# Kernel tuning notes

Hardware: AMD Instinct MI355X
Metric: run time of the kernel (lower is better)

Reference implementation:

```python
import jax, jax.numpy as jnp
import numpy as np

DOF = 7
DT = 0.1
MAX_VEL = 20.0
ACTION_RANGE = 50.0
BATCH = 16384


def skew(w):
    x, y, z = w[..., 0], w[..., 1], w[..., 2]
    o = jnp.zeros_like(x)
    return jnp.stack([jnp.stack([o, -z, y], -1),
                      jnp.stack([z, o, -x], -1),
                      jnp.stack([-y, x, o], -1)], -2)


def exp6(xi):
    # xi: (..., 6) twist [omega, v] (angular first). General se(3) exponential.
    w, v = xi[..., :3], xi[..., 3:]
    th = jnp.linalg.norm(w, axis=-1)                     # (...)
    small = th < 1e-10
    th_s = jnp.where(small, 1.0, th)
    W = skew(w / th_s[..., None])
    W2 = W @ W
    s, c = jnp.sin(th), jnp.cos(th)
    I3 = jnp.eye(3, dtype=xi.dtype)
    R = I3 + s[..., None, None] * W + (1.0 - c)[..., None, None] * W2
    Gm = th[..., None, None] * I3 + (1.0 - c)[..., None, None] * W + (th - s)[..., None, None] * W2
    p = jnp.einsum('...ij,...j->...i', Gm, v / th_s[..., None])
    R = jnp.where(small[..., None, None], I3, R)
    p = jnp.where(small[..., None], v, p)
    top = jnp.concatenate([R, p[..., None]], -1)
    bot = jnp.broadcast_to(jnp.array([0., 0., 0., 1.], xi.dtype), top.shape[:-2] + (1, 4))
    return jnp.concatenate([top, bot], -2)


def trans_inv(T):
    R = T[..., :3, :3]
    p = T[..., :3, 3]
    Rt = jnp.swapaxes(R, -1, -2)
    pi = -jnp.einsum('...ij,...j->...i', Rt, p)
    top = jnp.concatenate([Rt, pi[..., None]], -1)
    bot = jnp.broadcast_to(jnp.array([0., 0., 0., 1.], T.dtype), top.shape[:-2] + (1, 4))
    return jnp.concatenate([top, bot], -2)


def adjoint(T):
    R = T[..., :3, :3]
    p = T[..., :3, 3]
    pR = skew(p) @ R
    z = jnp.zeros_like(R)
    return jnp.concatenate([jnp.concatenate([R, z], -1),
                            jnp.concatenate([pR, R], -1)], -2)


def ad(V):
    w, v = V[..., :3], V[..., 3:]
    W, Vm = skew(w), skew(v)
    z = jnp.zeros_like(W)
    return jnp.concatenate([jnp.concatenate([W, z], -1),
                            jnp.concatenate([Vm, W], -1)], -2)


def inverse_dynamics(q, dq, ddq, gravity, ftip, Mlist, Glist, A):
    # Newton-Euler inverse dynamics (Modern Robotics), batched over B.
    B, n = q.shape
    dt = q.dtype
    V = jnp.zeros((B, 6), dt)
    Vd = jnp.concatenate([jnp.zeros((B, 3), dt), -jnp.broadcast_to(gravity, (B, 3))], -1)
    AdTs, Vs, Vds = [], [], []
    for i in range(n):  # forward recursion over joints (small fixed dof)
        Ti = exp6(-A[i] * q[:, i, None]) @ trans_inv(Mlist[i])   # (B,4,4)
        AdTi = adjoint(Ti)                                       # (B,6,6)
        V = jnp.einsum('bij,bj->bi', AdTi, V) + A[i] * dq[:, i, None]
        Vd = (jnp.einsum('bij,bj->bi', AdTi, Vd) + A[i] * ddq[:, i, None]
              + jnp.einsum('bij,j->bi', ad(V), A[i]) * dq[:, i, None])
        AdTs.append(AdTi)
        Vs.append(V)
        Vds.append(Vd)
    AdTs.append(jnp.broadcast_to(adjoint(trans_inv(Mlist[n])), (B, 6, 6)))
    F = jnp.broadcast_to(ftip, (B, 6))
    taus = [None] * n
    for i in range(n - 1, -1, -1):  # backward recursion
        GV = jnp.einsum('ij,bj->bi', Glist[i], Vs[i])
        F = (jnp.einsum('bji,bj->bi', AdTs[i + 1], F)
             + jnp.einsum('ij,bj->bi', Glist[i], Vds[i])
             - jnp.einsum('bji,bj->bi', ad(Vs[i]), GV))
        taus[i] = jnp.sum(F * A[i], -1)
    return jnp.stack(taus, -1)  # (B, n)


def forward_dynamics(q, dq, tau, gravity, ftip, Mlist, Glist, A):
    n = q.shape[1]
    z = jnp.zeros_like(q)
    g0 = jnp.zeros(3, q.dtype)
    f0 = jnp.zeros(6, q.dtype)
    # mass matrix columns via unit-ddq inverse dynamics
    cols = jax.vmap(lambda e: inverse_dynamics(q, z, jnp.broadcast_to(e, q.shape),
                                               g0, f0, Mlist, Glist, A))(jnp.eye(n, dtype=q.dtype))
    Mmat = jnp.transpose(cols, (1, 2, 0))                        # (B,n,n)
    # coriolis + gravity + end-effector bias in one pass (ddq=0)
    h = inverse_dynamics(q, dq, z, gravity, ftip, Mlist, Glist, A)
    return jnp.linalg.solve(Mmat, (tau - h)[..., None])[..., 0]


def _forward(state, torque, M_param, A, G_param, gravity, ftip):
    n = DOF
    # M property: keep top 3 rows, force bottom row to [0,0,0,1]
    bot = jnp.broadcast_to(jnp.array([0., 0., 0., 1.], M_param.dtype), (n + 1, 1, 4))
    Mlist = jnp.concatenate([M_param[:, :3], bot], axis=1)       # (n+1,4,4)
    # G property: diag(Ixx,Iyy,Izz,m,m,m)
    dvec = jnp.concatenate([G_param[:, :3], jnp.repeat(G_param[:, 3:4], 3, axis=1)], -1)
    Glist = dvec[:, :, None] * jnp.eye(6, dtype=G_param.dtype)   # (n,6,6)
    tau = torque * ACTION_RANGE

    def derivs(s, t):
        qpos, qvel, qf = s[..., :n], s[..., n:2 * n], s[..., 2 * n:3 * n]
        qacc = forward_dynamics(qpos, qvel, qf, gravity, ftip, Mlist, Glist, A)
        return jnp.concatenate([qvel, qacc, jnp.zeros_like(qf)], -1)

    s0 = jnp.concatenate([state, tau], -1)
    dt = DT
    k1 = derivs(s0, 0.0)
    k2 = derivs(s0 + 0.5 * dt * k1, 0.5 * dt)
    k3 = derivs(s0 + 0.5 * dt * k2, 0.5 * dt)
    k4 = derivs(s0 + dt * k3, dt)
    s1 = s0 + (dt / 6.0) * (k1 + 2.0 * k2 + 2.0 * k3 + k4)
    ns = s1[..., :2 * n]
    q = (ns[..., :n] + jnp.pi) % (2.0 * jnp.pi) - jnp.pi
    dq = jnp.clip(ns[..., n:], -MAX_VEL, MAX_VEL)
    # fk_in_space: chain link transforms, last frame is end-effector
    B = q.shape[0]
    T = jnp.broadcast_to(jnp.eye(4, dtype=q.dtype), (B, 4, 4))
    for i in range(n):
        T = T @ Mlist[i] @ exp6(A[i] * q[:, i, None])
    T = T @ Mlist[n]
    ee = T[:, :3, 3]
    return jnp.concatenate([q, dq], -1), ee


def setup_inputs() -> dict:
    key = jax.random.key(0)
    ks = jax.random.split(key, 6)
    state = jax.random.normal(ks[0], (BATCH, 2 * DOF), jnp.float32)
    torque = jax.random.normal(ks[1], (BATCH, DOF), jnp.float32)
    M_param = jnp.eye(4, dtype=jnp.float32)[None] + 0.05 * jax.random.normal(ks[2], (DOF + 1, 4, 4), jnp.float32)
    A = jax.random.uniform(ks[3], (DOF, 6), jnp.float32)
    G_param = jax.random.uniform(ks[4], (DOF, 4), jnp.float32, minval=0.1, maxval=1.0)
    gravity = jnp.array([0.0, -9.8, 0.0], jnp.float32)
    ftip = jnp.zeros(6, jnp.float32)
    return {"state": state, "torque": torque, "M_param": M_param, "A": A,
            "G_param": G_param, "gravity": gravity, "ftip": ftip}


def reference(state, torque, M_param, A, G_param, gravity, ftip):
    return _forward(state, torque, M_param, A, G_param, gravity, ftip)
```

## Files before the change

kernel.cpp:

```cpp
#include <hip/hip_runtime.h>
#include <math.h>

#define NB 16384

struct SConsts {
  float MrT[8][9];
  float mp[8][3];
  float A[7][6];
  float Gd[7][6];
  float X7p[3];
  float g[3];
  float ftip[6];
};

__device__ __forceinline__ void syncw() {
  __builtin_amdgcn_sched_barrier(0);
  __builtin_amdgcn_wave_barrier();
  __builtin_amdgcn_sched_barrier(0);
}

__device__ __forceinline__ float dot6(const float* a, const float* b) {
  return a[0]*b[0]+a[1]*b[1]+a[2]*b[2]+a[3]*b[3]+a[4]*b[4]+a[5]*b[5];
}

__device__ __forceinline__ void exp6_dev(float wx, float wy, float wz,
                                         float vx, float vy, float vz,
                                         float R[9], float p[3]) {
  float th2 = wx*wx + wy*wy + wz*wz;
  float th  = __builtin_amdgcn_sqrtf(th2);
  bool sm = th < 1e-10f;
  float ths = sm ? 1.0f : th;
  float inv = __builtin_amdgcn_rcpf(ths);
  float ux = wx*inv, uy = wy*inv, uz = wz*inv;
  float s = __sinf(th);
  float c = __cosf(th);
  float omc = 1.0f - c;
  float r00 = c + omc*ux*ux;
  float r01 = omc*ux*uy - s*uz;
  float r02 = omc*ux*uz + s*uy;
  float r10 = omc*uy*ux + s*uz;
  float r11 = c + omc*uy*uy;
  float r12 = omc*uy*uz - s*ux;
  float r20 = omc*uz*ux - s*uy;
  float r21 = omc*uz*uy + s*ux;
  float r22 = c + omc*uz*uz;
  float k1 = omc*inv, k2 = (th - s)*inv;
  float cx = uy*vz - uz*vy, cy = uz*vx - ux*vz, cz = ux*vy - uy*vx;
  float udv = ux*vx + uy*vy + uz*vz;
  float px = vx + k1*cx + k2*(ux*udv - vx);
  float py = vy + k1*cy + k2*(uy*udv - vy);
  float pz = vz + k1*cz + k2*(uz*udv - vz);
  R[0]=sm?1.f:r00; R[1]=sm?0.f:r01; R[2]=sm?0.f:r02;
  R[3]=sm?0.f:r10; R[4]=sm?1.f:r11; R[5]=sm?0.f:r12;
  R[6]=sm?0.f:r20; R[7]=sm?0.f:r21; R[8]=sm?1.f:r22;
  p[0]=sm?vx:px; p[1]=sm?vy:py; p[2]=sm?vz:pz;
}

__device__ __forceinline__ void Xapply(const float* R, const float* p,
                                       const float in[6], float out[6]) {
  float a = R[0]*in[0]+R[1]*in[1]+R[2]*in[2];
  float b = R[3]*in[0]+R[4]*in[1]+R[5]*in[2];
  float c = R[6]*in[0]+R[7]*in[1]+R[8]*in[2];
  float d = R[0]*in[3]+R[1]*in[4]+R[2]*in[5];
  float e = R[3]*in[3]+R[4]*in[4]+R[5]*in[5];
  float f = R[6]*in[3]+R[7]*in[4]+R[8]*in[5];
  out[0]=a; out[1]=b; out[2]=c;
  out[3] = p[1]*c - p[2]*b + d;
  out[4] = p[2]*a - p[0]*c + e;
  out[5] = p[0]*b - p[1]*a + f;
}

__device__ __forceinline__ void XTapply(const float* R, const float* p,
                                        const float in[6], float out[6]) {
  float fx=in[3], fy=in[4], fz=in[5];
  float tx = in[0] - (p[1]*fz - p[2]*fy);
  float ty = in[1] - (p[2]*fx - p[0]*fz);
  float tz = in[2] - (p[0]*fy - p[1]*fx);
  out[0] = R[0]*tx + R[3]*ty + R[6]*tz;
  out[1] = R[1]*tx + R[4]*ty + R[7]*tz;
  out[2] = R[2]*tx + R[5]*ty + R[8]*tz;
  out[3] = R[0]*fx + R[3]*fy + R[6]*fz;
  out[4] = R[1]*fx + R[4]*fy + R[7]*fz;
  out[5] = R[2]*fx + R[5]*fy + R[8]*fz;
}

extern "C" __global__ void __launch_bounds__(64, 2)
arm_kernel(const float* __restrict__ state, const float* __restrict__ torque,
           const float* __restrict__ Mp, const float* __restrict__ Ain,
           const float* __restrict__ Gp, const float* __restrict__ grav,
           const float* __restrict__ ftip_in, float* __restrict__ out)
{
  __shared__ SConsts C;
  __shared__ float XL[8][100];
  __shared__ float CL[8][68];
  const int t = threadIdx.x;

  {
    int i = t >> 3;
    #pragma unroll
    for (int kk = (t & 7); kk < 12; kk += 8) {
      if (kk < 9) {
        int r = kk / 3, c = kk - 3*(kk/3);
        C.MrT[i][c*3 + r] = Mp[i*16 + r*4 + c];
      } else {
        int r = kk - 9;
        C.mp[i][r] = Mp[i*16 + r*4 + 3];
      }
    }
    if (t < 42) {
      int i2 = t / 6, k = t - 6*(t/6);
      C.A[i2][k] = Ain[t];
      C.Gd[i2][k] = (k < 3) ? Gp[i2*4 + k] : Gp[i2*4 + 3];
    }
    if (t < 3) C.g[t] = grav[t];
    if (t < 6) C.ftip[t] = ftip_in[t];
  }
  syncw();
  if (t < 3)
    C.X7p[t] = -(C.MrT[7][t*3+0]*C.mp[7][0] + C.MrT[7][t*3+1]*C.mp[7][1] + C.MrT[7][t*3+2]*C.mp[7][2]);
  syncw();

  const int sub = t & 7;
  const int e   = t >> 3;
  const int b   = blockIdx.x * 8 + e;
  const int subc = (sub < 7) ? sub : 6;

  float dq0[7], tau[7], dqs[7];
  #pragma unroll
  for (int k = 0; k < 7; ++k) {
    dq0[k] = state[b*14 + 7 + k];
    tau[k] = torque[b*7 + k] * 50.0f;
    dqs[k] = dq0[k];
  }
  float q0s  = state[b*14 + subc];
  float dq0s = dq0[0];
  #pragma unroll
  for (int k = 1; k < 7; ++k) dq0s = (subc == k) ? dq0[k] : dq0s;

  float qss = q0s, dqss = dq0s;
  float accqs = 0.0f, accdqs = 0.0f;
  float a[7];
  const float gm = (sub == 7) ? 1.0f : 0.0f;

  #pragma unroll 1
  for (int stage = 0; stage < 4; ++stage) {
    syncw();
    if (sub < 7) {
      float Re[9], pe[3];
      exp6_dev(-C.A[sub][0]*qss, -C.A[sub][1]*qss, -C.A[sub][2]*qss,
               -C.A[sub][3]*qss, -C.A[sub][4]*qss, -C.A[sub][5]*qss, Re, pe);
      float Xr[12];
      #pragma unroll
      for (int r = 0; r < 3; ++r) {
        #pragma unroll
        for (int c = 0; c < 3; ++c)
          Xr[r*3+c] = Re[r*3+0]*C.MrT[sub][0+c] + Re[r*3+1]*C.MrT[sub][3+c] + Re[r*3+2]*C.MrT[sub][6+c];
      }
      #pragma unroll
      for (int r = 0; r < 3; ++r)
        Xr[9+r] = pe[r] - (Xr[r*3+0]*C.mp[sub][0] + Xr[r*3+1]*C.mp[sub][1] + Xr[r*3+2]*C.mp[sub][2]);
      float4* dst = (float4*)&XL[e][sub*12];
      dst[0] = make_float4(Xr[0],Xr[1],Xr[2],Xr[3]);
      dst[1] = make_float4(Xr[4],Xr[5],Xr[6],Xr[7]);
      dst[2] = make_float4(Xr[8],Xr[9],Xr[10],Xr[11]);
    }
    syncw();

    float X[7][12];
    #pragma unroll
    for (int i = 0; i < 7; ++i) {
      const float4* sx = (const float4*)&XL[e][i*12];
      float4 x0 = sx[0], x1 = sx[1], x2 = sx[2];
      X[i][0]=x0.x; X[i][1]=x0.y; X[i][2]=x0.z; X[i][3]=x0.w;
      X[i][4]=x1.x; X[i][5]=x1.y; X[i][6]=x1.z; X[i][7]=x1.w;
      X[i][8]=x2.x; X[i][9]=x2.y; X[i][10]=x2.z; X[i][11]=x2.w;
    }

    float V[6] = {0,0,0,0,0,0};
    float Vd[6];
    Vd[0]=0.0f; Vd[1]=0.0f; Vd[2]=0.0f;
    Vd[3] = -gm*C.g[0]; Vd[4] = -gm*C.g[1]; Vd[5] = -gm*C.g[2];
    float Fb[7][6];
    #pragma unroll
    for (int i = 0; i < 7; ++i) {
      float dqi  = (sub == 7) ? dqs[i] : 0.0f;
      float ddqi = (sub == i) ? 1.0f : 0.0f;
      float tv[6];
      Xapply(X[i], X[i]+9, V, tv);
      #pragma unroll
      for (int k = 0; k < 6; ++k) V[k] = tv[k] + C.A[i][k]*dqi;
      Xapply(X[i], X[i]+9, Vd, tv);
      float wx=V[0],wy=V[1],wz=V[2],vx=V[3],vy=V[4],vz=V[5];
      float ax=C.A[i][0],ay=C.A[i][1],az=C.A[i][2];
      float bx=C.A[i][3],by=C.A[i][4],bz=C.A[i][5];
      Vd[0] = tv[0] + ax*ddqi + (wy*az - wz*ay)*dqi;
      Vd[1] = tv[1] + ay*ddqi + (wz*ax - wx*az)*dqi;
      Vd[2] = tv[2] + az*ddqi + (wx*ay - wy*ax)*dqi;
      Vd[3] = tv[3] + bx*ddqi + (vy*az - vz*ay + wy*bz - wz*by)*dqi;
      Vd[4] = tv[4] + by*ddqi + (vz*ax - vx*az + wz*bx - wx*bz)*dqi;
      Vd[5] = tv[5] + bz*ddqi + (vx*ay - vy*ax + wx*by - wy*bx)*dqi;
      float g0=C.Gd[i][0], g1=C.Gd[i][1], g2=C.Gd[i][2], m=C.Gd[i][3];
      float Gt0=g0*wx, Gt1=g1*wy, Gt2=g2*wz;
      float Gb0=m*vx,  Gb1=m*vy,  Gb2=m*vz;
      Fb[i][0] = g0*Vd[0] + (wy*Gt2 - wz*Gt1) + (vy*Gb2 - vz*Gb1);
      Fb[i][1] = g1*Vd[1] + (wz*Gt0 - wx*Gt2) + (vz*Gb0 - vx*Gb2);
      Fb[i][2] = g2*Vd[2] + (wx*Gt1 - wy*Gt0) + (vx*Gb1 - vy*Gb0);
      Fb[i][3] = m*Vd[3] + (wy*Gb2 - wz*Gb1);
      Fb[i][4] = m*Vd[4] + (wz*Gb0 - wx*Gb2);
      Fb[i][5] = m*Vd[5] + (wx*Gb1 - wy*Gb0);
    }
    float col[7];
    float F[6];
    #pragma unroll
    for (int k = 0; k < 6; ++k) F[k] = gm*C.ftip[k];
    #pragma unroll
    for (int i = 6; i >= 0; --i) {
      float tv[6];
      if (i == 6) XTapply(C.MrT[7], C.X7p, F, tv);
      else        XTapply(X[i+1], X[i+1]+9, F, tv);
      #pragma unroll
      for (int k = 0; k < 6; ++k) F[k] = tv[k] + Fb[i][k];
      col[i] = dot6(F, C.A[i]);
    }

    syncw();
    #pragma unroll
    for (int k = 0; k < 7; ++k) CL[e][k*8 + sub] = col[k];
    syncw();
    float Mm[7][7], rhs[7];
    #pragma unroll
    for (int i = 0; i < 7; ++i) {
      const float4* rp = (const float4*)&CL[e][i*8];
      float4 r0 = rp[0], r1 = rp[1];
      Mm[i][0]=r0.x; Mm[i][1]=r0.y; Mm[i][2]=r0.z; Mm[i][3]=r0.w;
      Mm[i][4]=r1.x; Mm[i][5]=r1.y; Mm[i][6]=r1.z;
      rhs[i] = tau[i] - r1.w;
    }

    float invd[7];
    #pragma unroll
    for (int k = 0; k < 7; ++k) {
      invd[k] = __builtin_amdgcn_rcpf(Mm[k][k]);
      #pragma unroll
      for (int i2 = k+1; i2 < 7; ++i2) {
        float f = Mm[i2][k] * invd[k];
        #pragma unroll
        for (int c2 = k+1; c2 < 7; ++c2) Mm[i2][c2] -= f * Mm[k][c2];
        rhs[i2] -= f * rhs[k];
      }
    }
    #pragma unroll
    for (int i2 = 6; i2 >= 0; --i2) {
      float s = rhs[i2];
      #pragma unroll
      for (int c2 = i2+1; c2 < 7; ++c2) s -= Mm[i2][c2] * a[c2];
      a[i2] = s * invd[i2];
    }

    float a_own = a[0];
    #pragma unroll
    for (int k = 1; k < 7; ++k) a_own = (subc == k) ? a[k] : a_own;
    float w = (stage == 1 || stage == 2) ? 2.0f : 1.0f;
    accqs  += w*dqss;
    accdqs += w*a_own;
    if (stage < 3) {
      float cc = (stage == 2) ? 0.1f : 0.05f;
      qss  = q0s + cc*dqss;
      dqss = dq0s + cc*a_own;
      #pragma unroll
      for (int k = 0; k < 7; ++k) dqs[k] = dq0[k] + cc*a[k];
    }
  }

  const float c6 = (float)(0.1/6.0);
  const float PI_F = 3.14159265358979323846f;
  const float TWO_PI_F = 6.28318530717958647692f;
  const float INV_TWO_PI_F = 0.15915494309189535f;
  float q1 = q0s  + c6*accqs;
  float d1 = dq0s + c6*accdqs;
  float x = q1 + PI_F;
  float n = floorf(x * INV_TWO_PI_F);
  float y = fmaf(n, -TWO_PI_F, x);
  y = (y < 0.0f) ? y + TWO_PI_F : y;
  y = (y >= TWO_PI_F) ? y - TWO_PI_F : y;
  float qw_own  = y - PI_F;
  float dqw_own = fminf(fmaxf(d1, -20.0f), 20.0f);
  if (sub < 7) {
    out[b*14 + sub]     = qw_own;
    out[b*14 + 7 + sub] = dqw_own;
  }

  syncw();
  if (sub < 7) {
    float Re[9], pe[3];
    exp6_dev(C.A[sub][0]*qw_own, C.A[sub][1]*qw_own, C.A[sub][2]*qw_own,
             C.A[sub][3]*qw_own, C.A[sub][4]*qw_own, C.A[sub][5]*qw_own, Re, pe);
    float L[12];
    #pragma unroll
    for (int r = 0; r < 3; ++r) {
      #pragma unroll
      for (int c = 0; c < 3; ++c)
        L[r*3+c] = C.MrT[sub][0*3+r]*Re[0*3+c] + C.MrT[sub][1*3+r]*Re[1*3+c] + C.MrT[sub][2*3+r]*Re[2*3+c];
      L[9+r] = C.MrT[sub][0*3+r]*pe[0] + C.MrT[sub][1*3+r]*pe[1] + C.MrT[sub][2*3+r]*pe[2] + C.mp[sub][r];
    }
    float4* dst = (float4*)&XL[e][sub*12];
    dst[0] = make_float4(L[0],L[1],L[2],L[3]);
    dst[1] = make_float4(L[4],L[5],L[6],L[7]);
    dst[2] = make_float4(L[8],L[9],L[10],L[11]);
  }
  syncw();
  float X2[7][12];
  #pragma unroll
  for (int i = 0; i < 7; ++i) {
    const float4* sx = (const float4*)&XL[e][i*12];
    float4 x0 = sx[0], x1 = sx[1], x2 = sx[2];
    X2[i][0]=x0.x; X2[i][1]=x0.y; X2[i][2]=x0.z; X2[i][3]=x0.w;
    X2[i][4]=x1.x; X2[i][5]=x1.y; X2[i][6]=x1.z; X2[i][7]=x1.w;
    X2[i][8]=x2.x; X2[i][9]=x2.y; X2[i][10]=x2.z; X2[i][11]=x2.w;
  }
  float v0 = C.mp[7][0], v1 = C.mp[7][1], v2 = C.mp[7][2];
  #pragma unroll
  for (int i = 6; i >= 0; --i) {
    float n0 = X2[i][0]*v0 + X2[i][1]*v1 + X2[i][2]*v2 + X2[i][9];
    float n1 = X2[i][3]*v0 + X2[i][4]*v1 + X2[i][5]*v2 + X2[i][10];
    float n2 = X2[i][6]*v0 + X2[i][7]*v1 + X2[i][8]*v2 + X2[i][11];
    v0 = n0; v1 = n1; v2 = n2;
  }
  {
    float ev = v0;
    ev = (sub == 1) ? v1 : ev;
    ev = (sub == 2) ? v2 : ev;
    if (sub < 3) out[NB*14 + b*3 + sub] = ev;
  }
}

extern "C" void kernel_launch(void* const* d_in, const int* in_sizes, int n_in,
                              void* d_out, int out_size, void* d_ws, size_t ws_size,
                              hipStream_t stream) {
  const float* state  = (const float*)d_in[0];
  const float* torque = (const float*)d_in[1];
  const float* Mp     = (const float*)d_in[2];
  const float* Ain    = (const float*)d_in[3];
  const float* Gp     = (const float*)d_in[4];
  const float* grav   = (const float*)d_in[5];
  const float* ftip   = (const float*)d_in[6];
  float* out = (float*)d_out;
  hipLaunchKernelGGL(arm_kernel, dim3(NB/8), dim3(64), 0, stream,
                     state, torque, Mp, Ain, Gp, grav, ftip, out);
}
```

Measured before the change: 26.53 us.

## Map each arm column to its own wavefront with 64 batch elements per block

Restructures the thread mapping so that each of 8 wavefronts handles one mass-matrix column (or the bias term) for 64 batch elements. Before, 8 lanes of one wave cooperated on a single element. Because every lane in a wave now takes the same path, the column waves can run a specialised cheaper recursion that drops the velocity terms, and only wave 7 runs the full Newton-Euler with gravity and velocities. Divergent per-lane masking goes away, but the change brings block-wide __syncthreads, larger LDS use (about 47KB), and more per-wave register pressure. The end-effector FK now runs on one wave only.

After: 30.60 us. 15.3% more time.

```diff
diff --git a/kernel.cpp b/kernel.cpp
--- a/kernel.cpp
+++ b/kernel.cpp
@@ -2,6 +2,7 @@
 #include <math.h>
 
 #define NB 16384
+#define ESTR 92
 
 struct SConsts {
   float MrT[8][9];
@@ -12,12 +13,6 @@
   float g[3];
   float ftip[6];
 };
-
-__device__ __forceinline__ void syncw() {
-  __builtin_amdgcn_sched_barrier(0);
-  __builtin_amdgcn_wave_barrier();
-  __builtin_amdgcn_sched_barrier(0);
-}
 
 __device__ __forceinline__ float dot6(const float* a, const float* b) {
   return a[0]*b[0]+a[1]*b[1]+a[2]*b[2]+a[3]*b[3]+a[4]*b[4]+a[5]*b[5];
@@ -84,18 +79,65 @@
   out[5] = R[2]*fx + R[5]*fy + R[8]*fz;
 }
 
-extern "C" __global__ void __launch_bounds__(64, 2)
+__device__ __forceinline__ void build_X(const SConsts& C, int j, float q,
+                                        float* dstp) {
+  float Re[9], pe[3];
+  exp6_dev(-C.A[j][0]*q, -C.A[j][1]*q, -C.A[j][2]*q,
+           -C.A[j][3]*q, -C.A[j][4]*q, -C.A[j][5]*q, Re, pe);
+  float Xr[12];
+  #pragma unroll
+  for (int r = 0; r < 3; ++r) {
+    #pragma unroll
+    for (int c = 0; c < 3; ++c)
+      Xr[r*3+c] = Re[r*3+0]*C.MrT[j][0+c] + Re[r*3+1]*C.MrT[j][3+c] + Re[r*3+2]*C.MrT[j][6+c];
+  }
+  #pragma unroll
+  for (int r = 0; r < 3; ++r)
+    Xr[9+r] = pe[r] - (Xr[r*3+0]*C.mp[j][0] + Xr[r*3+1]*C.mp[j][1] + Xr[r*3+2]*C.mp[j][2]);
+  float4* dst = (float4*)dstp;
+  dst[0] = make_float4(Xr[0],Xr[1],Xr[2],Xr[3]);
+  dst[1] = make_float4(Xr[4],Xr[5],Xr[6],Xr[7]);
+  dst[2] = make_float4(Xr[8],Xr[9],Xr[10],Xr[11]);
+}
+
+__device__ __forceinline__ void solve7(float Mm[7][7], float rhs[7], float a[7]) {
+  float invd[7];
+  #pragma unroll
+  for (int k = 0; k < 7; ++k) {
+    invd[k] = __builtin_amdgcn_rcpf(Mm[k][k]);
+    #pragma unroll
+    for (int i2 = k+1; i2 < 7; ++i2) {
+      float f = Mm[i2][k] * invd[k];
+      #pragma unroll
+      for (int c2 = k+1; c2 < 7; ++c2) Mm[i2][c2] -= f * Mm[k][c2];
+      rhs[i2] -= f * rhs[k];
+    }
+  }
+  #pragma unroll
+  for (int i2 = 6; i2 >= 0; --i2) {
+    float s = rhs[i2];
+    #pragma unroll
+    for (int c2 = i2+1; c2 < 7; ++c2) s -= Mm[i2][c2] * a[c2];
+    a[i2] = s * invd[i2];
+  }
+}
+
+extern "C" __global__ void __launch_bounds__(512, 2)
 arm_kernel(const float* __restrict__ state, const float* __restrict__ torque,
            const float* __restrict__ Mp, const float* __restrict__ Ain,
            const float* __restrict__ Gp, const float* __restrict__ grav,
            const float* __restrict__ ftip_in, float* __restrict__ out)
 {
   __shared__ SConsts C;
-  __shared__ float XL[8][100];
-  __shared__ float CL[8][68];
+  __shared__ float XL[64*ESTR];
+  __shared__ float CL[64*ESTR];
   const int t = threadIdx.x;
-
-  {
+  const int w = t >> 6;
+  const int l = t & 63;
+  const int b = blockIdx.x * 64 + l;
+  const int wc = (w < 7) ? w : 6;
+
+  if (t < 64) {
     int i = t >> 3;
     #pragma unroll
     for (int kk = (t & 7); kk < 12; kk += 8) {
@@ -115,100 +157,89 @@
     if (t < 3) C.g[t] = grav[t];
     if (t < 6) C.ftip[t] = ftip_in[t];
   }
-  syncw();
+  __syncthreads();
   if (t < 3)
     C.X7p[t] = -(C.MrT[7][t*3+0]*C.mp[7][0] + C.MrT[7][t*3+1]*C.mp[7][1] + C.MrT[7][t*3+2]*C.mp[7][2]);
-  syncw();
-
-  const int sub = t & 7;
-  const int e   = t >> 3;
-  const int b   = blockIdx.x * 8 + e;
-  const int subc = (sub < 7) ? sub : 6;
-
-  float dq0[7], tau[7], dqs[7];
-  #pragma unroll
-  for (int k = 0; k < 7; ++k) {
-    dq0[k] = state[b*14 + 7 + k];
-    tau[k] = torque[b*7 + k] * 50.0f;
-    dqs[k] = dq0[k];
-  }
-  float q0s  = state[b*14 + subc];
-  float dq0s = dq0[0];
-  #pragma unroll
-  for (int k = 1; k < 7; ++k) dq0s = (subc == k) ? dq0[k] : dq0s;
+
+  float tau[7];
+  #pragma unroll
+  for (int k = 0; k < 7; ++k) tau[k] = torque[b*7 + k] * 50.0f;
+  float q0s  = state[b*14 + wc];
+  float dq0s = state[b*14 + 7 + wc];
+  float dq0[7], dqs[7];
+  if (w == 7) {
+    #pragma unroll
+    for (int k = 0; k < 7; ++k) { dq0[k] = state[b*14 + 7 + k]; dqs[k] = dq0[k]; }
+  }
 
   float qss = q0s, dqss = dq0s;
-  float accqs = 0.0f, accdqs = 0.0f;
+  float accq = 0.0f, accdq = 0.0f;
   float a[7];
-  const float gm = (sub == 7) ? 1.0f : 0.0f;
+  const float gm = (w == 7) ? 1.0f : 0.0f;
 
   #pragma unroll 1
   for (int stage = 0; stage < 4; ++stage) {
-    syncw();
-    if (sub < 7) {
-      float Re[9], pe[3];
-      exp6_dev(-C.A[sub][0]*qss, -C.A[sub][1]*qss, -C.A[sub][2]*qss,
-               -C.A[sub][3]*qss, -C.A[sub][4]*qss, -C.A[sub][5]*qss, Re, pe);
-      float Xr[12];
-      #pragma unroll
-      for (int r = 0; r < 3; ++r) {
-        #pragma unroll
-        for (int c = 0; c < 3; ++c)
-          Xr[r*3+c] = Re[r*3+0]*C.MrT[sub][0+c] + Re[r*3+1]*C.MrT[sub][3+c] + Re[r*3+2]*C.MrT[sub][6+c];
-      }
-      #pragma unroll
-      for (int r = 0; r < 3; ++r)
-        Xr[9+r] = pe[r] - (Xr[r*3+0]*C.mp[sub][0] + Xr[r*3+1]*C.mp[sub][1] + Xr[r*3+2]*C.mp[sub][2]);
-      float4* dst = (float4*)&XL[e][sub*12];
-      dst[0] = make_float4(Xr[0],Xr[1],Xr[2],Xr[3]);
-      dst[1] = make_float4(Xr[4],Xr[5],Xr[6],Xr[7]);
-      dst[2] = make_float4(Xr[8],Xr[9],Xr[10],Xr[11]);
-    }
-    syncw();
+    if (w < 7) build_X(C, w, qss, &XL[l*ESTR + w*12]);
+    __syncthreads();
 
     float X[7][12];
     #pragma unroll
     for (int i = 0; i < 7; ++i) {
-      const float4* sx = (const float4*)&XL[e][i*12];
+      const float4* sx = (const float4*)&XL[l*ESTR + i*12];
       float4 x0 = sx[0], x1 = sx[1], x2 = sx[2];
       X[i][0]=x0.x; X[i][1]=x0.y; X[i][2]=x0.z; X[i][3]=x0.w;
       X[i][4]=x1.x; X[i][5]=x1.y; X[i][6]=x1.z; X[i][7]=x1.w;
       X[i][8]=x2.x; X[i][9]=x2.y; X[i][10]=x2.z; X[i][11]=x2.w;
     }
 
-    float V[6] = {0,0,0,0,0,0};
-    float Vd[6];
-    Vd[0]=0.0f; Vd[1]=0.0f; Vd[2]=0.0f;
-    Vd[3] = -gm*C.g[0]; Vd[4] = -gm*C.g[1]; Vd[5] = -gm*C.g[2];
     float Fb[7][6];
-    #pragma unroll
-    for (int i = 0; i < 7; ++i) {
-      float dqi  = (sub == 7) ? dqs[i] : 0.0f;
-      float ddqi = (sub == i) ? 1.0f : 0.0f;
-      float tv[6];
-      Xapply(X[i], X[i]+9, V, tv);
-      #pragma unroll
-      for (int k = 0; k < 6; ++k) V[k] = tv[k] + C.A[i][k]*dqi;
-      Xapply(X[i], X[i]+9, Vd, tv);
-      float wx=V[0],wy=V[1],wz=V[2],vx=V[3],vy=V[4],vz=V[5];
-      float ax=C.A[i][0],ay=C.A[i][1],az=C.A[i][2];
-      float bx=C.A[i][3],by=C.A[i][4],bz=C.A[i][5];
-      Vd[0] = tv[0] + ax*ddqi + (wy*az - wz*ay)*dqi;
-      Vd[1] = tv[1] + ay*ddqi + (wz*ax - wx*az)*dqi;
-      Vd[2] = tv[2] + az*ddqi + (wx*ay - wy*ax)*dqi;
-      Vd[3] = tv[3] + bx*ddqi + (vy*az - vz*ay + wy*bz - wz*by)*dqi;
-      Vd[4] = tv[4] + by*ddqi + (vz*ax - vx*az + wz*bx - wx*bz)*dqi;
-      Vd[5] = tv[5] + bz*ddqi + (vx*ay - vy*ax + wx*by - wy*bx)*dqi;
-      float g0=C.Gd[i][0], g1=C.Gd[i][1], g2=C.Gd[i][2], m=C.Gd[i][3];
-      float Gt0=g0*wx, Gt1=g1*wy, Gt2=g2*wz;
-      float Gb0=m*vx,  Gb1=m*vy,  Gb2=m*vz;
-      Fb[i][0] = g0*Vd[0] + (wy*Gt2 - wz*Gt1) + (vy*Gb2 - vz*Gb1);
-      Fb[i][1] = g1*Vd[1] + (wz*Gt0 - wx*Gt2) + (vz*Gb0 - vx*Gb2);
-      Fb[i][2] = g2*Vd[2] + (wx*Gt1 - wy*Gt0) + (vx*Gb1 - vy*Gb0);
-      Fb[i][3] = m*Vd[3] + (wy*Gb2 - wz*Gb1);
-      Fb[i][4] = m*Vd[4] + (wz*Gb0 - wx*Gb2);
-      Fb[i][5] = m*Vd[5] + (wx*Gb1 - wy*Gb0);
-    }
+    if (w == 7) {
+      float V[6] = {0,0,0,0,0,0};
+      float Vd[6];
+      Vd[0]=0.0f; Vd[1]=0.0f; Vd[2]=0.0f;
+      Vd[3] = -C.g[0]; Vd[4] = -C.g[1]; Vd[5] = -C.g[2];
+      #pragma unroll
+      for (int i = 0; i < 7; ++i) {
+        float dqi = dqs[i];
+        float tv[6];
+        Xapply(X[i], X[i]+9, V, tv);
+        #pragma unroll
+        for (int k = 0; k < 6; ++k) V[k] = tv[k] + C.A[i][k]*dqi;
+        Xapply(X[i], X[i]+9, Vd, tv);
+        float wx=V[0],wy=V[1],wz=V[2],vx=V[3],vy=V[4],vz=V[5];
+        float ax=C.A[i][0],ay=C.A[i][1],az=C.A[i][2];
+        float bx=C.A[i][3],by=C.A[i][4],bz=C.A[i][5];
+        Vd[0] = tv[0] + (wy*az - wz*ay)*dqi;
+        Vd[1] = tv[1] + (wz*ax - wx*az)*dqi;
+        Vd[2] = tv[2] + (wx*ay - wy*ax)*dqi;
+        Vd[3] = tv[3] + (vy*az - vz*ay + wy*bz - wz*by)*dqi;
+        Vd[4] = tv[4] + (vz*ax - vx*az + wz*bx - wx*bz)*dqi;
+        Vd[5] = tv[5] + (vx*ay - vy*ax + wx*by - wy*bx)*dqi;
+        float g0=C.Gd[i][0], g1=C.Gd[i][1], g2=C.Gd[i][2], m=C.Gd[i][3];
+        float Gt0=g0*wx, Gt1=g1*wy, Gt2=g2*wz;
+        float Gb0=m*vx,  Gb1=m*vy,  Gb2=m*vz;
+        Fb[i][0] = g0*Vd[0] + (wy*Gt2 - wz*Gt1) + (vy*Gb2 - vz*Gb1);
+        Fb[i][1] = g1*Vd[1] + (wz*Gt0 - wx*Gt2) + (vz*Gb0 - vx*Gb2);
+        Fb[i][2] = g2*Vd[2] + (wx*Gt1 - wy*Gt0) + (vx*Gb1 - vy*Gb0);
+        Fb[i][3] = m*Vd[3] + (wy*Gb2 - wz*Gb1);
+        Fb[i][4] = m*Vd[4] + (wz*Gb0 - wx*Gb2);
+        Fb[i][5] = m*Vd[5] + (wx*Gb1 - wy*Gb0);
+      }
+    } else {
+      float Vd[6] = {0,0,0,0,0,0};
+      #pragma unroll
+      for (int i = 0; i < 7; ++i) {
+        float tv[6];
+        Xapply(X[i], X[i]+9, Vd, tv);
+        float ddqi = (i == w) ? 1.0f : 0.0f;
+        #pragma unroll
+        for (int k = 0; k < 6; ++k) {
+          Vd[k] = tv[k] + C.A[i][k]*ddqi;
+          Fb[i][k] = C.Gd[i][k]*Vd[k];
+        }
+      }
+    }
+
     float col[7];
     float F[6];
     #pragma unroll
@@ -223,52 +254,35 @@
       col[i] = dot6(F, C.A[i]);
     }
 
-    syncw();
-    #pragma unroll
-    for (int k = 0; k < 7; ++k) CL[e][k*8 + sub] = col[k];
-    syncw();
+    #pragma unroll
+    for (int k = 0; k < 7; ++k) CL[l*ESTR + k*12 + w] = col[k];
+    __syncthreads();
+
     float Mm[7][7], rhs[7];
     #pragma unroll
     for (int i = 0; i < 7; ++i) {
-      const float4* rp = (const float4*)&CL[e][i*8];
+      const float4* rp = (const float4*)&CL[l*ESTR + i*12];
       float4 r0 = rp[0], r1 = rp[1];
       Mm[i][0]=r0.x; Mm[i][1]=r0.y; Mm[i][2]=r0.z; Mm[i][3]=r0.w;
       Mm[i][4]=r1.x; Mm[i][5]=r1.y; Mm[i][6]=r1.z;
       rhs[i] = tau[i] - r1.w;
     }
-
-    float invd[7];
-    #pragma unroll
-    for (int k = 0; k < 7; ++k) {
-      invd[k] = __builtin_amdgcn_rcpf(Mm[k][k]);
-      #pragma unroll
-      for (int i2 = k+1; i2 < 7; ++i2) {
-        float f = Mm[i2][k] * invd[k];
-        #pragma unroll
-        for (int c2 = k+1; c2 < 7; ++c2) Mm[i2][c2] -= f * Mm[k][c2];
-        rhs[i2] -= f * rhs[k];
-      }
-    }
-    #pragma unroll
-    for (int i2 = 6; i2 >= 0; --i2) {
-      float s = rhs[i2];
-      #pragma unroll
-      for (int c2 = i2+1; c2 < 7; ++c2) s -= Mm[i2][c2] * a[c2];
-      a[i2] = s * invd[i2];
-    }
+    solve7(Mm, rhs, a);
 
     float a_own = a[0];
     #pragma unroll
-    for (int k = 1; k < 7; ++k) a_own = (subc == k) ? a[k] : a_own;
-    float w = (stage == 1 || stage == 2) ? 2.0f : 1.0f;
-    accqs  += w*dqss;
-    accdqs += w*a_own;
+    for (int k = 1; k < 7; ++k) a_own = (wc == k) ? a[k] : a_own;
+    float wgt = (stage == 1 || stage == 2) ? 2.0f : 1.0f;
+    accq  += wgt*dqss;
+    accdq += wgt*a_own;
     if (stage < 3) {
       float cc = (stage == 2) ? 0.1f : 0.05f;
       qss  = q0s + cc*dqss;
       dqss = dq0s + cc*a_own;
-      #pragma unroll
-      for (int k = 0; k < 7; ++k) dqs[k] = dq0[k] + cc*a[k];
+      if (w == 7) {
+        #pragma unroll
+        for (int k = 0; k < 7; ++k) dqs[k] = dq0[k] + cc*a[k];
+      }
     }
   }
 
@@ -276,8 +290,8 @@
   const float PI_F = 3.14159265358979323846f;
   const float TWO_PI_F = 6.28318530717958647692f;
   const float INV_TWO_PI_F = 0.15915494309189535f;
-  float q1 = q0s  + c6*accqs;
-  float d1 = dq0s + c6*accdqs;
+  float q1 = q0s  + c6*accq;
+  float d1 = dq0s + c6*accdq;
   float x = q1 + PI_F;
   float n = floorf(x * INV_TWO_PI_F);
   float y = fmaf(n, -TWO_PI_F, x);
@@ -285,52 +299,43 @@
   y = (y >= TWO_PI_F) ? y - TWO_PI_F : y;
   float qw_own  = y - PI_F;
   float dqw_own = fminf(fmaxf(d1, -20.0f), 20.0f);
-  if (sub < 7) {
-    out[b*14 + sub]     = qw_own;
-    out[b*14 + 7 + sub] = dqw_own;
-  }
-
-  syncw();
-  if (sub < 7) {
+  if (w < 7) {
+    out[b*14 + w]     = qw_own;
+    out[b*14 + 7 + w] = dqw_own;
+  }
+
+  if (w < 7) {
     float Re[9], pe[3];
-    exp6_dev(C.A[sub][0]*qw_own, C.A[sub][1]*qw_own, C.A[sub][2]*qw_own,
-             C.A[sub][3]*qw_own, C.A[sub][4]*qw_own, C.A[sub][5]*qw_own, Re, pe);
+    exp6_dev(C.A[w][0]*qw_own, C.A[w][1]*qw_own, C.A[w][2]*qw_own,
+             C.A[w][3]*qw_own, C.A[w][4]*qw_own, C.A[w][5]*qw_own, Re, pe);
     float L[12];
     #pragma unroll
     for (int r = 0; r < 3; ++r) {
       #pragma unroll
       for (int c = 0; c < 3; ++c)
-        L[r*3+c] = C.MrT[sub][0*3+r]*Re[0*3+c] + C.MrT[sub][1*3+r]*Re[1*3+c] + C.MrT[sub][2*3+r]*Re[2*3+c];
-      L[9+r] = C.MrT[sub][0*3+r]*pe[0] + C.MrT[sub][1*3+r]*pe[1] + C.MrT[sub][2*3+r]*pe[2] + C.mp[sub][r];
-    }
-    float4* dst = (float4*)&XL[e][sub*12];
+        L[r*3+c] = C.MrT[w][0*3+r]*Re[0*3+c] + C.MrT[w][1*3+r]*Re[1*3+c] + C.MrT[w][2*3+r]*Re[2*3+c];
+      L[9+r] = C.MrT[w][0*3+r]*pe[0] + C.MrT[w][1*3+r]*pe[1] + C.MrT[w][2*3+r]*pe[2] + C.mp[w][r];
+    }
+    float4* dst = (float4*)&XL[l*ESTR + w*12];
     dst[0] = make_float4(L[0],L[1],L[2],L[3]);
     dst[1] = make_float4(L[4],L[5],L[6],L[7]);
     dst[2] = make_float4(L[8],L[9],L[10],L[11]);
   }
-  syncw();
-  float X2[7][12];
-  #pragma unroll
-  for (int i = 0; i < 7; ++i) {
-    const float4* sx = (const float4*)&XL[e][i*12];
-    float4 x0 = sx[0], x1 = sx[1], x2 = sx[2];
-    X2[i][0]=x0.x; X2[i][1]=x0.y; X2[i][2]=x0.z; X2[i][3]=x0.w;
-    X2[i][4]=x1.x; X2[i][5]=x1.y; X2[i][6]=x1.z; X2[i][7]=x1.w;
-    X2[i][8]=x2.x; X2[i][9]=x2.y; X2[i][10]=x2.z; X2[i][11]=x2.w;
-  }
-  float v0 = C.mp[7][0], v1 = C.mp[7][1], v2 = C.mp[7][2];
-  #pragma unroll
-  for (int i = 6; i >= 0; --i) {
-    float n0 = X2[i][0]*v0 + X2[i][1]*v1 + X2[i][2]*v2 + X2[i][9];
-    float n1 = X2[i][3]*v0 + X2[i][4]*v1 + X2[i][5]*v2 + X2[i][10];
-    float n2 = X2[i][6]*v0 + X2[i][7]*v1 + X2[i][8]*v2 + X2[i][11];
-    v0 = n0; v1 = n1; v2 = n2;
-  }
-  {
-    float ev = v0;
-    ev = (sub == 1) ? v1 : ev;
-    ev = (sub == 2) ? v2 : ev;
-    if (sub < 3) out[NB*14 + b*3 + sub] = ev;
+  __syncthreads();
+  if (w == 7) {
+    float v0 = C.mp[7][0], v1 = C.mp[7][1], v2 = C.mp[7][2];
+    #pragma unroll
+    for (int i = 6; i >= 0; --i) {
+      const float4* sx = (const float4*)&XL[l*ESTR + i*12];
+      float4 x0 = sx[0], x1 = sx[1], x2 = sx[2];
+      float n0 = x0.x*v0 + x0.y*v1 + x0.z*v2 + x2.y;
+      float n1 = x0.w*v0 + x1.x*v1 + x1.y*v2 + x2.z;
+      float n2 = x1.z*v0 + x1.w*v1 + x2.x*v2 + x2.w;
+      v0 = n0; v1 = n1; v2 = n2;
+    }
+    out[NB*14 + b*3 + 0] = v0;
+    out[NB*14 + b*3 + 1] = v1;
+    out[NB*14 + b*3 + 2] = v2;
   }
 }
 
@@ -345,6 +350,6 @@
   const float* grav   = (const float*)d_in[5];
   const float* ftip   = (const float*)d_in[6];
   float* out = (float*)d_out;
-  hipLaunchKernelGGL(arm_kernel, dim3(NB/8), dim3(64), 0, stream,
+  hipLaunchKernelGGL(arm_kernel, dim3(NB/64), dim3(512), 0, stream,
                      state, torque, Mp, Ain, Gp, grav, ftip, out);
 }
```
